# Optimization experiments

Hardware: AMD Instinct MI355X
Metric: run time of the kernel (lower is better)

## Reference

```python
import jax, jax.numpy as jnp
import numpy as np

D_MODEL = 256
N_HEAD = 8


def setup_inputs() -> dict:
    key = jax.random.key(0)
    ks = jax.random.split(key, 9)
    B, S, D = 2, 2048, D_MODEL
    s = 1.0 / np.sqrt(D)
    return {
        "x": jax.random.normal(ks[0], (B, S, D), dtype=jnp.float32),
        "wq": jax.random.uniform(ks[1], (D, D), jnp.float32, -s, s),
        "bq": jax.random.uniform(ks[2], (D,), jnp.float32, -s, s),
        "wk": jax.random.uniform(ks[3], (D, D), jnp.float32, -s, s),
        "bk": jax.random.uniform(ks[4], (D,), jnp.float32, -s, s),
        "wv": jax.random.uniform(ks[5], (D, D), jnp.float32, -s, s),
        "bv": jax.random.uniform(ks[6], (D,), jnp.float32, -s, s),
        "wc": jax.random.uniform(ks[7], (D, D), jnp.float32, -s, s),
        "bc": jax.random.uniform(ks[8], (D,), jnp.float32, -s, s),
    }


def _split_heads(t):
    # [B, S, D] -> [B, H, S, D/H]
    B, S, D = t.shape
    return t.reshape(B, S, N_HEAD, D // N_HEAD).transpose(0, 2, 1, 3)


def reference(x, wq, bq, wk, bk, wv, bv, wc, bc):
    q = _split_heads(x @ wq.T + bq)
    k = _split_heads(x @ wk.T + bk)
    v = _split_heads(x @ wv.T + bv)
    d_head = q.shape[-1]
    # full [B, H, S, S] score matrix, as in the original (non-fused)
    score = jnp.einsum("bhqd,bhkd->bhqk", q, k) / jnp.sqrt(jnp.float32(d_head))
    attn = jax.nn.softmax(score, axis=-1)
    out = jnp.einsum("bhqk,bhkd->bhqd", attn, v)
    B, H, S, Dh = out.shape
    out = out.transpose(0, 2, 1, 3).reshape(B, S, H * Dh)
    out = out @ wc.T + bc
    attention = jnp.mean(attn, axis=1)  # [B, S, S]
    return (out, attention)
```

## Files before the change

kernel.cpp:

```cpp
#include <hip/hip_runtime.h>
#include <hip/hip_bf16.h>


#define B_   2
#define S_   2048
#define D_   256
#define H_   8
#define DH_  32
#define NROW (B_*S_)
#define KSPLIT 4
#define KKEYS (S_/KSPLIT)

typedef __attribute__((ext_vector_type(8))) short bf16x8;
typedef __attribute__((ext_vector_type(4))) float f32x4;

__device__ __forceinline__ f32x4 mfma_bf16(bf16x8 a, bf16x8 b, f32x4 c) {
    return __builtin_amdgcn_mfma_f32_16x16x32_bf16(a, b, c, 0, 0, 0);
}

__device__ __forceinline__ float fast_exp2(float x) {
    return __builtin_amdgcn_exp2f(x);
}

__device__ __forceinline__ unsigned short f2bf_bits(float v) {
    __hip_bfloat16 h = __float2bfloat16(v);
    return *reinterpret_cast<unsigned short*>(&h);
}

__device__ __forceinline__ size_t fragidx(int m, int k) {
    return (size_t)(m >> 4) * 4096 + (k >> 5) * 512 + ((k >> 3) & 3) * 128
           + (m & 15) * 8 + (k & 7);
}

__global__ void split_all(const float4* __restrict__ x,
                          const float4* __restrict__ wq, const float4* __restrict__ wk,
                          const float4* __restrict__ wv, const float4* __restrict__ wc,
                          ushort4* __restrict__ xh, ushort4* __restrict__ xl,
                          ushort4* __restrict__ wqh, ushort4* __restrict__ wql,
                          ushort4* __restrict__ wkh, ushort4* __restrict__ wkl,
                          ushort4* __restrict__ wvh, ushort4* __restrict__ wvl,
                          ushort4* __restrict__ wch, ushort4* __restrict__ wcl) {
    int i = blockIdx.x * 256 + threadIdx.x;
    const float4* src; ushort4 *ph, *pl; int off;
    if (i < 262144) { src = x; ph = xh; pl = xl; off = i; }
    else {
        int j = i - 262144;
        int rg = j >> 14; off = j & 16383;
        if (rg == 0)      { src = wq; ph = wqh; pl = wql; }
        else if (rg == 1) { src = wk; ph = wkh; pl = wkl; }
        else if (rg == 2) { src = wv; ph = wvh; pl = wvl; }
        else              { src = wc; ph = wch; pl = wcl; }
    }
    float4 v = src[off];
    float vv[4] = {v.x, v.y, v.z, v.w};
    ushort4 hb, lb;
    unsigned short* hp = (unsigned short*)&hb;
    unsigned short* lp = (unsigned short*)&lb;
    for (int c = 0; c < 4; c++) {
        __hip_bfloat16 h = __float2bfloat16(vv[c]);
        hp[c] = *reinterpret_cast<unsigned short*>(&h);
        lp[c] = f2bf_bits(vv[c] - __bfloat162float(h));
    }
    int m = off >> 6, k = (off & 63) * 4;
    size_t fi = fragidx(m, k);
    ph[fi >> 2] = hb;
    pl[fi >> 2] = lb;
}

__global__ __launch_bounds__(256) void qkv_gemm(
    const __hip_bfloat16* __restrict__ xh, const __hip_bfloat16* __restrict__ xl,
    const __hip_bfloat16* __restrict__ w0h, const __hip_bfloat16* __restrict__ w0l,
    const __hip_bfloat16* __restrict__ w1h, const __hip_bfloat16* __restrict__ w1l,
    const __hip_bfloat16* __restrict__ w2h, const __hip_bfloat16* __restrict__ w2l,
    const float* __restrict__ bq, const float* __restrict__ bk, const float* __restrict__ bvv,
    __hip_bfloat16* __restrict__ Qf, __hip_bfloat16* __restrict__ Kf,
    __hip_bfloat16* __restrict__ Vf)
{
    int z = blockIdx.z;
    const __hip_bfloat16* wh = (z==0) ? w0h : (z==1) ? w1h : w2h;
    const __hip_bfloat16* wl = (z==0) ? w0l : (z==1) ? w1l : w2l;
    const float* bias = (z==0) ? bq : (z==1) ? bk : bvv;
    const float sv = (z==0) ? 0.17677669529663687f * 1.4426950408889634f : 1.0f;

    int tid = threadIdx.x;
    int w = tid >> 6, lid = tid & 63, quad = lid >> 4, l15 = lid & 15;
    int row0 = blockIdx.x * 64 + (w >> 1) * 32;
    int col0 = blockIdx.y * 64 + (w & 1) * 32;

    f32x4 acc[2][2] = {};
#pragma unroll
    for (int k0 = 0; k0 < 256; k0 += 32) {
        bf16x8 ah[2], al[2], bh[2], bl[2];
        for (int mi = 0; mi < 2; mi++) {
            size_t ro = (size_t)((row0 + mi * 16) >> 4) * 4096 + (k0 >> 5) * 512 + lid * 8;
            ah[mi] = *(const bf16x8*)(xh + ro);
            al[mi] = *(const bf16x8*)(xl + ro);
        }
        for (int ni = 0; ni < 2; ni++) {
            size_t co = (size_t)((col0 + ni * 16) >> 4) * 4096 + (k0 >> 5) * 512 + lid * 8;
            bh[ni] = *(const bf16x8*)(wh + co);
            bl[ni] = *(const bf16x8*)(wl + co);
        }
        for (int mi = 0; mi < 2; mi++)
            for (int ni = 0; ni < 2; ni++) {
                acc[mi][ni] = mfma_bf16(ah[mi], bh[ni], acc[mi][ni]);
                acc[mi][ni] = mfma_bf16(ah[mi], bl[ni], acc[mi][ni]);
                acc[mi][ni] = mfma_bf16(al[mi], bh[ni], acc[mi][ni]);
            }
    }
    for (int mi = 0; mi < 2; mi++)
        for (int ni = 0; ni < 2; ni++) {
            int col = col0 + ni * 16 + l15;
            int h = col >> 5, dh = col & 31;
            float bvl = bias[col];
            for (int r = 0; r < 4; r++) {
                int row = row0 + mi * 16 + quad * 4 + r;
                int b = row >> 11, s = row & 2047;
                __hip_bfloat16 o = __float2bfloat16((acc[mi][ni][r] + bvl) * sv);
                size_t bh_base = (size_t)(b * H_ + h) * (S_ * DH_);
                if (z == 2) {
                    int oo = s & 31;
                    int slot = ((oo & 15) >> 2) * 8 + ((oo >> 4) << 2) + (oo & 3);
                    Vf[bh_base + (s >> 5) * 1024 + (dh >> 4) * 512
                       + (slot >> 3) * 128 + (dh & 15) * 8 + (slot & 7)] = o;
                } else {
                    size_t idx = bh_base + (s >> 4) * 512 + (dh >> 3) * 128
                                 + (s & 15) * 8 + (dh & 7);
                    if (z == 0) Qf[idx] = o; else Kf[idx] = o;
                }
            }
        }
}

__global__ __launch_bounds__(256) void attn_flash(
    const __hip_bfloat16* __restrict__ Qf, const __hip_bfloat16* __restrict__ Kf,
    const __hip_bfloat16* __restrict__ Vf,
    float* __restrict__ Opart, float* __restrict__ Lpart)
{
    int tid = threadIdx.x, w = tid >> 6, lid = tid & 63, quad = lid >> 4, l15 = lid & 15;
    int h = blockIdx.y;
    int b = blockIdx.z >> 2, ks = blockIdx.z & 3;
    int q0 = (blockIdx.x * 4 + w) * 16;
    size_t bh_base = (size_t)(b * H_ + h) * (S_ * DH_);
    const __hip_bfloat16* Qp = Qf + bh_base + (q0 >> 4) * 512 + lid * 8;
    const __hip_bfloat16* Kp = Kf + bh_base + lid * 8;
    const __hip_bfloat16* Vp = Vf + bh_base + lid * 8;
    bf16x8 qf = *(const bf16x8*)Qp;
    f32x4 zacc = {};
    f32x4 oacc[2] = {};
    float lp0 = 0.f, lp1 = 0.f;

    int kbeg = ks * KKEYS;
    bf16x8 kf0 = *(const bf16x8*)(Kp + (kbeg >> 4) * 512);
    bf16x8 kf1 = *(const bf16x8*)(Kp + (kbeg >> 4) * 512 + 512);
    bf16x8 vf0 = *(const bf16x8*)(Vp + (kbeg >> 5) * 1024);
    bf16x8 vf1 = *(const bf16x8*)(Vp + (kbeg >> 5) * 1024 + 512);

#pragma unroll 2
    for (int k0 = kbeg; k0 < kbeg + KKEYS; k0 += 32) {
        bf16x8 ck0 = kf0, ck1 = kf1, cv0 = vf0, cv1 = vf1;
        int kn = (k0 + 32 < kbeg + KKEYS) ? k0 + 32 : kbeg;
        kf0 = *(const bf16x8*)(Kp + (kn >> 4) * 512);
        kf1 = *(const bf16x8*)(Kp + (kn >> 4) * 512 + 512);
        vf0 = *(const bf16x8*)(Vp + (kn >> 5) * 1024);
        vf1 = *(const bf16x8*)(Vp + (kn >> 5) * 1024 + 512);

        __builtin_amdgcn_s_setprio(1);
        f32x4 c0 = mfma_bf16(ck0, qf, zacc);
        f32x4 c1 = mfma_bf16(ck1, qf, zacc);
        __builtin_amdgcn_s_setprio(0);
        float e0[4], e1[4];
        for (int r = 0; r < 4; r++) {
            e0[r] = fast_exp2(c0[r]);
            e1[r] = fast_exp2(c1[r]);
        }
        lp0 += e0[0] + e0[1] + e0[2] + e0[3];
        lp1 += e1[0] + e1[1] + e1[2] + e1[3];
        union { bf16x8 v; __hip_bfloat162 h2[4]; } pu;
        pu.h2[0] = __float22bfloat162_rn(make_float2(e0[0], e0[1]));
        pu.h2[1] = __float22bfloat162_rn(make_float2(e0[2], e0[3]));
        pu.h2[2] = __float22bfloat162_rn(make_float2(e1[0], e1[1]));
        pu.h2[3] = __float22bfloat162_rn(make_float2(e1[2], e1[3]));
        __builtin_amdgcn_s_setprio(1);
        oacc[0] = mfma_bf16(cv0, pu.v, oacc[0]);
        oacc[1] = mfma_bf16(cv1, pu.v, oacc[1]);
        __builtin_amdgcn_s_setprio(0);
    }
    float lp = lp0 + lp1;
    lp += __shfl_xor(lp, 16);
    lp += __shfl_xor(lp, 32);

    size_t base = (size_t)((b * H_ + h) * KSPLIT + ks) * S_;
    if (lid < 16) Lpart[base + q0 + lid] = lp;
    f32x4* op = (f32x4*)(Opart + (base + q0 + l15) * DH_);
    op[quad] = oacc[0];
    op[quad + 4] = oacc[1];
}

__global__ __launch_bounds__(256) void attn_combine(
    const float* __restrict__ Opart, const float* __restrict__ Lpart,
    __hip_bfloat16* __restrict__ cth, __hip_bfloat16* __restrict__ ctl,
    float* __restrict__ invL)
{
    int i = blockIdx.x * 256 + threadIdx.x;
    int dh = i & 31;
    int s = (i >> 5) & (S_ - 1);
    int hb = i >> 16;
    float l = 0.f, o = 0.f;
#pragma unroll
    for (int ks = 0; ks < KSPLIT; ks++) {
        size_t base = (size_t)(hb * KSPLIT + ks) * S_ + s;
        l += Lpart[base];
        o += Opart[base * DH_ + dh];
    }
    float inv = 1.0f / l;
    float val = o * inv;
    int b = hb >> 3, h = hb & 7;
    size_t fi = fragidx(b * S_ + s, h * DH_ + dh);
    __hip_bfloat16 hv = __float2bfloat16(val);
    cth[fi] = hv;
    ctl[fi] = __float2bfloat16(val - __bfloat162float(hv));
    if (dh == 0) invL[hb * S_ + s] = inv;
}

__global__ __launch_bounds__(256) void attn_write(
    const __hip_bfloat16* __restrict__ Qf, const __hip_bfloat16* __restrict__ Kf,
    const float* __restrict__ invL, float* __restrict__ attn)
{
    __shared__ float invbuf[H_ * 16];
    int tid = threadIdx.x, w = tid >> 6, lid = tid & 63, quad = lid >> 4, l15 = lid & 15;
    int b = blockIdx.z;
    int q0 = blockIdx.y * 16;
    int k0 = blockIdx.x * 256 + w * 64;
    if (tid < 128) {
        int h = tid >> 4, r = tid & 15;
        invbuf[tid] = invL[(b * H_ + h) * S_ + q0 + r] * 0.125f;
    }
    __syncthreads();
    f32x4 zacc = {};
    float psum[4][4] = {};
    size_t bh0 = (size_t)b * H_ * (S_ * DH_);
    size_t qoff = (size_t)(q0 >> 4) * 512 + lid * 8;
    size_t koff = (size_t)(k0 >> 4) * 512 + lid * 8;

    bf16x8 qcur = *(const bf16x8*)(Qf + bh0 + qoff);
    bf16x8 kcur0 = *(const bf16x8*)(Kf + bh0 + koff);
    bf16x8 kcur1 = *(const bf16x8*)(Kf + bh0 + koff + 512);
    bf16x8 kcur2 = *(const bf16x8*)(Kf + bh0 + koff + 1024);
    bf16x8 kcur3 = *(const bf16x8*)(Kf + bh0 + koff + 1536);

#pragma unroll 2
    for (int h = 0; h < H_; h++) {
        int hn = (h < H_ - 1) ? h + 1 : h;
        size_t nb = bh0 + (size_t)hn * (S_ * DH_);
        bf16x8 qn = *(const bf16x8*)(Qf + nb + qoff);
        bf16x8 kn0 = *(const bf16x8*)(Kf + nb + koff);
        bf16x8 kn1 = *(const bf16x8*)(Kf + nb + koff + 512);
        bf16x8 kn2 = *(const bf16x8*)(Kf + nb + koff + 1024);
        bf16x8 kn3 = *(const bf16x8*)(Kf + nb + koff + 1536);

        float il[4];
        for (int r = 0; r < 4; r++) il[r] = invbuf[h * 16 + quad * 4 + r];

        __builtin_amdgcn_s_setprio(1);
        f32x4 c0 = mfma_bf16(qcur, kcur0, zacc);
        f32x4 c1 = mfma_bf16(qcur, kcur1, zacc);
        f32x4 c2 = mfma_bf16(qcur, kcur2, zacc);
        f32x4 c3 = mfma_bf16(qcur, kcur3, zacc);
        __builtin_amdgcn_s_setprio(0);
        for (int r = 0; r < 4; r++) {
            psum[0][r] += fast_exp2(c0[r]) * il[r];
            psum[1][r] += fast_exp2(c1[r]) * il[r];
            psum[2][r] += fast_exp2(c2[r]) * il[r];
            psum[3][r] += fast_exp2(c3[r]) * il[r];
        }
        qcur = qn;
        kcur0 = kn0; kcur1 = kn1; kcur2 = kn2; kcur3 = kn3;
    }
    for (int nt = 0; nt < 4; nt++)
        for (int r = 0; r < 4; r++)
            attn[(size_t)(b * S_ + q0 + quad * 4 + r) * S_ + k0 + nt * 16 + l15] =
                psum[nt][r];
}

__global__ __launch_bounds__(256) void out_gemm(
    const __hip_bfloat16* __restrict__ ch, const __hip_bfloat16* __restrict__ cl,
    const __hip_bfloat16* __restrict__ wh, const __hip_bfloat16* __restrict__ wl,
    const float* __restrict__ bias, float* __restrict__ out)
{
    int tid = threadIdx.x;
    int w = tid >> 6, lid = tid & 63, quad = lid >> 4, l15 = lid & 15;
    int row0 = blockIdx.x * 64 + (w >> 1) * 32;
    int col0 = blockIdx.y * 64 + (w & 1) * 32;

    f32x4 acc[2][2] = {};
#pragma unroll
    for (int k0 = 0; k0 < 256; k0 += 32) {
        bf16x8 ah[2], al[2], bh[2], bl[2];
        for (int mi = 0; mi < 2; mi++) {
            size_t ro = (size_t)((row0 + mi * 16) >> 4) * 4096 + (k0 >> 5) * 512 + lid * 8;
            ah[mi] = *(const bf16x8*)(ch + ro);
            al[mi] = *(const bf16x8*)(cl + ro);
        }
        for (int ni = 0; ni < 2; ni++) {
            size_t co = (size_t)((col0 + ni * 16) >> 4) * 4096 + (k0 >> 5) * 512 + lid * 8;
            bh[ni] = *(const bf16x8*)(wh + co);
            bl[ni] = *(const bf16x8*)(wl + co);
        }
        for (int mi = 0; mi < 2; mi++)
            for (int ni = 0; ni < 2; ni++) {
                acc[mi][ni] = mfma_bf16(ah[mi], bh[ni], acc[mi][ni]);
                acc[mi][ni] = mfma_bf16(ah[mi], bl[ni], acc[mi][ni]);
                acc[mi][ni] = mfma_bf16(al[mi], bh[ni], acc[mi][ni]);
            }
    }
    for (int mi = 0; mi < 2; mi++)
        for (int ni = 0; ni < 2; ni++) {
            int col = col0 + ni * 16 + l15;
            float bvl = bias[col];
            for (int r = 0; r < 4; r++) {
                int row = row0 + mi * 16 + quad * 4 + r;
                out[(size_t)row * 256 + col] = acc[mi][ni][r] + bvl;
            }
        }
}

extern "C" void kernel_launch(void* const* d_in, const int* in_sizes, int n_in,
                              void* d_out, int out_size, void* d_ws, size_t ws_size,
                              hipStream_t stream) {
    const float* x  = (const float*)d_in[0];
    const float* wq = (const float*)d_in[1];
    const float* bq = (const float*)d_in[2];
    const float* wk = (const float*)d_in[3];
    const float* bk = (const float*)d_in[4];
    const float* wv = (const float*)d_in[5];
    const float* bv = (const float*)d_in[6];
    const float* wc = (const float*)d_in[7];
    const float* bc = (const float*)d_in[8];

    char* ws = (char*)d_ws;
    const size_t MB = 1u << 20;
    const size_t KB128 = 128u * 1024u;
    __hip_bfloat16* xh  = (__hip_bfloat16*)(ws + 0 * MB);
    __hip_bfloat16* xl  = (__hip_bfloat16*)(ws + 2 * MB);
    __hip_bfloat16* wqh = (__hip_bfloat16*)(ws + 4 * MB + 0 * KB128);
    __hip_bfloat16* wql = (__hip_bfloat16*)(ws + 4 * MB + 1 * KB128);
    __hip_bfloat16* wkh = (__hip_bfloat16*)(ws + 4 * MB + 2 * KB128);
    __hip_bfloat16* wkl = (__hip_bfloat16*)(ws + 4 * MB + 3 * KB128);
    __hip_bfloat16* wvh = (__hip_bfloat16*)(ws + 4 * MB + 4 * KB128);
    __hip_bfloat16* wvl = (__hip_bfloat16*)(ws + 4 * MB + 5 * KB128);
    __hip_bfloat16* wch = (__hip_bfloat16*)(ws + 4 * MB + 6 * KB128);
    __hip_bfloat16* wcl = (__hip_bfloat16*)(ws + 4 * MB + 7 * KB128);
    __hip_bfloat16* Qfb = (__hip_bfloat16*)(ws + 5 * MB);
    __hip_bfloat16* Kfb = (__hip_bfloat16*)(ws + 7 * MB);
    __hip_bfloat16* Vfb = (__hip_bfloat16*)(ws + 9 * MB);
    __hip_bfloat16* cth = (__hip_bfloat16*)(ws + 11 * MB);
    __hip_bfloat16* ctl = (__hip_bfloat16*)(ws + 13 * MB);
    float* Opart = (float*)(ws + 15 * MB);
    float* Lpart = (float*)(ws + 31 * MB);
    float* invL  = (float*)(ws + 31 * MB + 512 * 1024);

    float* outp  = (float*)d_out;
    float* attnp = outp + (size_t)NROW * D_;

    hipLaunchKernelGGL(split_all, dim3(1280), dim3(256), 0, stream,
                       (const float4*)x, (const float4*)wq, (const float4*)wk,
                       (const float4*)wv, (const float4*)wc,
                       (ushort4*)xh, (ushort4*)xl,
                       (ushort4*)wqh, (ushort4*)wql, (ushort4*)wkh, (ushort4*)wkl,
                       (ushort4*)wvh, (ushort4*)wvl, (ushort4*)wch, (ushort4*)wcl);

    hipLaunchKernelGGL(qkv_gemm, dim3(NROW / 64, 4, 3), dim3(256), 0, stream,
                       xh, xl, wqh, wql, wkh, wkl, wvh, wvl, bq, bk, bv, Qfb, Kfb, Vfb);

    hipLaunchKernelGGL(attn_flash, dim3(S_ / 64, H_, B_ * KSPLIT), dim3(256), 0, stream,
                       Qfb, Kfb, Vfb, Opart, Lpart);

    hipLaunchKernelGGL(attn_combine, dim3(4096), dim3(256), 0, stream,
                       Opart, Lpart, cth, ctl, invL);

    hipLaunchKernelGGL(attn_write, dim3(S_ / 256, S_ / 16, B_), dim3(256), 0, stream,
                       Qfb, Kfb, invL, attnp);

    hipLaunchKernelGGL(out_gemm, dim3(NROW / 64, 4), dim3(256), 0, stream,
                       cth, ctl, wch, wcl, bc, outp);
}
```

Before: 142.4 us.

## Fuse split-K combine into flash kernel and merge attn-write with output GEMM

Each flash block now handles 16 queries with its four waves splitting the keys, and reduces the partial O and L through shared memory inside the block. This removes the Opart/Lpart global round trip and the separate combine kernel. The attention-map write and the output projection GEMM are merged into one launch by indexing on block ID, which cuts launch count and lets the two independent workloads overlap. The cost is a block-wide sync in the flash kernel and a heterogeneous grid whose two block types have different register needs.

```diff
diff --git a/kernel.cpp b/kernel.cpp
--- a/kernel.cpp
+++ b/kernel.cpp
@@ -135,12 +135,15 @@
 __global__ __launch_bounds__(256) void attn_flash(
     const __hip_bfloat16* __restrict__ Qf, const __hip_bfloat16* __restrict__ Kf,
     const __hip_bfloat16* __restrict__ Vf,
-    float* __restrict__ Opart, float* __restrict__ Lpart)
+    __hip_bfloat16* __restrict__ cth, __hip_bfloat16* __restrict__ ctl,
+    float* __restrict__ invL)
 {
+    __shared__ float sO[KSPLIT][16][33];
+    __shared__ float sL[KSPLIT][16];
     int tid = threadIdx.x, w = tid >> 6, lid = tid & 63, quad = lid >> 4, l15 = lid & 15;
     int h = blockIdx.y;
-    int b = blockIdx.z >> 2, ks = blockIdx.z & 3;
-    int q0 = (blockIdx.x * 4 + w) * 16;
+    int b = blockIdx.z;
+    int q0 = blockIdx.x * 16;
     size_t bh_base = (size_t)(b * H_ + h) * (S_ * DH_);
     const __hip_bfloat16* Qp = Qf + bh_base + (q0 >> 4) * 512 + lid * 8;
     const __hip_bfloat16* Kp = Kf + bh_base + lid * 8;
@@ -150,7 +153,7 @@
     f32x4 oacc[2] = {};
     float lp0 = 0.f, lp1 = 0.f;
 
-    int kbeg = ks * KKEYS;
+    int kbeg = w * KKEYS;
     bf16x8 kf0 = *(const bf16x8*)(Kp + (kbeg >> 4) * 512);
     bf16x8 kf1 = *(const bf16x8*)(Kp + (kbeg >> 4) * 512 + 512);
     bf16x8 vf0 = *(const bf16x8*)(Vp + (kbeg >> 5) * 1024);
@@ -190,139 +193,129 @@
     lp += __shfl_xor(lp, 16);
     lp += __shfl_xor(lp, 32);
 
-    size_t base = (size_t)((b * H_ + h) * KSPLIT + ks) * S_;
-    if (lid < 16) Lpart[base + q0 + lid] = lp;
-    f32x4* op = (f32x4*)(Opart + (base + q0 + l15) * DH_);
-    op[quad] = oacc[0];
-    op[quad + 4] = oacc[1];
-}
-
-__global__ __launch_bounds__(256) void attn_combine(
-    const float* __restrict__ Opart, const float* __restrict__ Lpart,
-    __hip_bfloat16* __restrict__ cth, __hip_bfloat16* __restrict__ ctl,
-    float* __restrict__ invL)
-{
-    int i = blockIdx.x * 256 + threadIdx.x;
-    int dh = i & 31;
-    int s = (i >> 5) & (S_ - 1);
-    int hb = i >> 16;
-    float l = 0.f, o = 0.f;
+    for (int r = 0; r < 4; r++) {
+        sO[w][l15][quad * 4 + r]      = oacc[0][r];
+        sO[w][l15][16 + quad * 4 + r] = oacc[1][r];
+    }
+    if (lid < 16) sL[w][lid] = lp;
+    __syncthreads();
+
+    int d = tid & 31, q = tid >> 5;
 #pragma unroll
-    for (int ks = 0; ks < KSPLIT; ks++) {
-        size_t base = (size_t)(hb * KSPLIT + ks) * S_ + s;
-        l += Lpart[base];
-        o += Opart[base * DH_ + dh];
-    }
-    float inv = 1.0f / l;
-    float val = o * inv;
-    int b = hb >> 3, h = hb & 7;
-    size_t fi = fragidx(b * S_ + s, h * DH_ + dh);
-    __hip_bfloat16 hv = __float2bfloat16(val);
-    cth[fi] = hv;
-    ctl[fi] = __float2bfloat16(val - __bfloat162float(hv));
-    if (dh == 0) invL[hb * S_ + s] = inv;
-}
-
-__global__ __launch_bounds__(256) void attn_write(
+    for (int qq = q; qq < 16; qq += 8) {
+        float l = sL[0][qq] + sL[1][qq] + sL[2][qq] + sL[3][qq];
+        float o = sO[0][qq][d] + sO[1][qq][d] + sO[2][qq][d] + sO[3][qq][d];
+        float inv = 1.0f / l;
+        float val = o * inv;
+        size_t fi = fragidx(b * S_ + q0 + qq, h * DH_ + d);
+        __hip_bfloat16 hv = __float2bfloat16(val);
+        cth[fi] = hv;
+        ctl[fi] = __float2bfloat16(val - __bfloat162float(hv));
+        if (d == 0) invL[(b * H_ + h) * S_ + q0 + qq] = inv;
+    }
+}
+
+__global__ __launch_bounds__(256) void attn_out(
     const __hip_bfloat16* __restrict__ Qf, const __hip_bfloat16* __restrict__ Kf,
-    const float* __restrict__ invL, float* __restrict__ attn)
+    const float* __restrict__ invL,
+    const __hip_bfloat16* __restrict__ ch, const __hip_bfloat16* __restrict__ cl,
+    const __hip_bfloat16* __restrict__ wh, const __hip_bfloat16* __restrict__ wl,
+    const float* __restrict__ bias,
+    float* __restrict__ attn, float* __restrict__ out)
 {
     __shared__ float invbuf[H_ * 16];
+    int bid = blockIdx.x;
     int tid = threadIdx.x, w = tid >> 6, lid = tid & 63, quad = lid >> 4, l15 = lid & 15;
-    int b = blockIdx.z;
-    int q0 = blockIdx.y * 16;
-    int k0 = blockIdx.x * 256 + w * 64;
-    if (tid < 128) {
-        int h = tid >> 4, r = tid & 15;
-        invbuf[tid] = invL[(b * H_ + h) * S_ + q0 + r] * 0.125f;
-    }
-    __syncthreads();
-    f32x4 zacc = {};
-    float psum[4][4] = {};
-    size_t bh0 = (size_t)b * H_ * (S_ * DH_);
-    size_t qoff = (size_t)(q0 >> 4) * 512 + lid * 8;
-    size_t koff = (size_t)(k0 >> 4) * 512 + lid * 8;
-
-    bf16x8 qcur = *(const bf16x8*)(Qf + bh0 + qoff);
-    bf16x8 kcur0 = *(const bf16x8*)(Kf + bh0 + koff);
-    bf16x8 kcur1 = *(const bf16x8*)(Kf + bh0 + koff + 512);
-    bf16x8 kcur2 = *(const bf16x8*)(Kf + bh0 + koff + 1024);
-    bf16x8 kcur3 = *(const bf16x8*)(Kf + bh0 + koff + 1536);
-
-#pragma unroll 2
-    for (int h = 0; h < H_; h++) {
-        int hn = (h < H_ - 1) ? h + 1 : h;
-        size_t nb = bh0 + (size_t)hn * (S_ * DH_);
-        bf16x8 qn = *(const bf16x8*)(Qf + nb + qoff);
-        bf16x8 kn0 = *(const bf16x8*)(Kf + nb + koff);
-        bf16x8 kn1 = *(const bf16x8*)(Kf + nb + koff + 512);
-        bf16x8 kn2 = *(const bf16x8*)(Kf + nb + koff + 1024);
-        bf16x8 kn3 = *(const bf16x8*)(Kf + nb + koff + 1536);
-
-        float il[4];
-        for (int r = 0; r < 4; r++) il[r] = invbuf[h * 16 + quad * 4 + r];
-
-        __builtin_amdgcn_s_setprio(1);
-        f32x4 c0 = mfma_bf16(qcur, kcur0, zacc);
-        f32x4 c1 = mfma_bf16(qcur, kcur1, zacc);
-        f32x4 c2 = mfma_bf16(qcur, kcur2, zacc);
-        f32x4 c3 = mfma_bf16(qcur, kcur3, zacc);
-        __builtin_amdgcn_s_setprio(0);
-        for (int r = 0; r < 4; r++) {
-            psum[0][r] += fast_exp2(c0[r]) * il[r];
-            psum[1][r] += fast_exp2(c1[r]) * il[r];
-            psum[2][r] += fast_exp2(c2[r]) * il[r];
-            psum[3][r] += fast_exp2(c3[r]) * il[r];
-        }
-        qcur = qn;
-        kcur0 = kn0; kcur1 = kn1; kcur2 = kn2; kcur3 = kn3;
-    }
-    for (int nt = 0; nt < 4; nt++)
-        for (int r = 0; r < 4; r++)
-            attn[(size_t)(b * S_ + q0 + quad * 4 + r) * S_ + k0 + nt * 16 + l15] =
-                psum[nt][r];
-}
-
-__global__ __launch_bounds__(256) void out_gemm(
-    const __hip_bfloat16* __restrict__ ch, const __hip_bfloat16* __restrict__ cl,
-    const __hip_bfloat16* __restrict__ wh, const __hip_bfloat16* __restrict__ wl,
-    const float* __restrict__ bias, float* __restrict__ out)
-{
-    int tid = threadIdx.x;
-    int w = tid >> 6, lid = tid & 63, quad = lid >> 4, l15 = lid & 15;
-    int row0 = blockIdx.x * 64 + (w >> 1) * 32;
-    int col0 = blockIdx.y * 64 + (w & 1) * 32;
-
-    f32x4 acc[2][2] = {};
+
+    if (bid < 256) {
+        int row0 = (bid & 63) * 64 + (w >> 1) * 32;
+        int col0 = (bid >> 6) * 64 + (w & 1) * 32;
+
+        f32x4 acc[2][2] = {};
 #pragma unroll
-    for (int k0 = 0; k0 < 256; k0 += 32) {
-        bf16x8 ah[2], al[2], bh[2], bl[2];
-        for (int mi = 0; mi < 2; mi++) {
-            size_t ro = (size_t)((row0 + mi * 16) >> 4) * 4096 + (k0 >> 5) * 512 + lid * 8;
-            ah[mi] = *(const bf16x8*)(ch + ro);
-            al[mi] = *(const bf16x8*)(cl + ro);
-        }
-        for (int ni = 0; ni < 2; ni++) {
-            size_t co = (size_t)((col0 + ni * 16) >> 4) * 4096 + (k0 >> 5) * 512 + lid * 8;
-            bh[ni] = *(const bf16x8*)(wh + co);
-            bl[ni] = *(const bf16x8*)(wl + co);
+        for (int k0 = 0; k0 < 256; k0 += 32) {
+            bf16x8 ah[2], al[2], bh[2], bl[2];
+            for (int mi = 0; mi < 2; mi++) {
+                size_t ro = (size_t)((row0 + mi * 16) >> 4) * 4096 + (k0 >> 5) * 512 + lid * 8;
+                ah[mi] = *(const bf16x8*)(ch + ro);
+                al[mi] = *(const bf16x8*)(cl + ro);
+            }
+            for (int ni = 0; ni < 2; ni++) {
+                size_t co = (size_t)((col0 + ni * 16) >> 4) * 4096 + (k0 >> 5) * 512 + lid * 8;
+                bh[ni] = *(const bf16x8*)(wh + co);
+                bl[ni] = *(const bf16x8*)(wl + co);
+            }
+            for (int mi = 0; mi < 2; mi++)
+                for (int ni = 0; ni < 2; ni++) {
+                    acc[mi][ni] = mfma_bf16(ah[mi], bh[ni], acc[mi][ni]);
+                    acc[mi][ni] = mfma_bf16(ah[mi], bl[ni], acc[mi][ni]);
+                    acc[mi][ni] = mfma_bf16(al[mi], bh[ni], acc[mi][ni]);
+                }
         }
         for (int mi = 0; mi < 2; mi++)
             for (int ni = 0; ni < 2; ni++) {
-                acc[mi][ni] = mfma_bf16(ah[mi], bh[ni], acc[mi][ni]);
-                acc[mi][ni] = mfma_bf16(ah[mi], bl[ni], acc[mi][ni]);
-                acc[mi][ni] = mfma_bf16(al[mi], bh[ni], acc[mi][ni]);
-            }
-    }
-    for (int mi = 0; mi < 2; mi++)
-        for (int ni = 0; ni < 2; ni++) {
-            int col = col0 + ni * 16 + l15;
-            float bvl = bias[col];
+                int col = col0 + ni * 16 + l15;
+                float bvl = bias[col];
+                for (int r = 0; r < 4; r++) {
+                    int row = row0 + mi * 16 + quad * 4 + r;
+                    out[(size_t)row * 256 + col] = acc[mi][ni][r] + bvl;
+                }
+            }
+    } else {
+        int ab = bid - 256;
+        int kx = ab & 7, qy = (ab >> 3) & 127, b = ab >> 10;
+        int q0 = qy * 16;
+        int k0 = kx * 256 + w * 64;
+        if (tid < 128) {
+            int h = tid >> 4, r = tid & 15;
+            invbuf[tid] = invL[(b * H_ + h) * S_ + q0 + r] * 0.125f;
+        }
+        __syncthreads();
+        f32x4 zacc = {};
+        float psum[4][4] = {};
+        size_t bh0 = (size_t)b * H_ * (S_ * DH_);
+        size_t qoff = (size_t)(q0 >> 4) * 512 + lid * 8;
+        size_t koff = (size_t)(k0 >> 4) * 512 + lid * 8;
+
+        bf16x8 qcur = *(const bf16x8*)(Qf + bh0 + qoff);
+        bf16x8 kcur0 = *(const bf16x8*)(Kf + bh0 + koff);
+        bf16x8 kcur1 = *(const bf16x8*)(Kf + bh0 + koff + 512);
+        bf16x8 kcur2 = *(const bf16x8*)(Kf + bh0 + koff + 1024);
+        bf16x8 kcur3 = *(const bf16x8*)(Kf + bh0 + koff + 1536);
+
+#pragma unroll 2
+        for (int h = 0; h < H_; h++) {
+            int hn = (h < H_ - 1) ? h + 1 : h;
+            size_t nb = bh0 + (size_t)hn * (S_ * DH_);
+            bf16x8 qn = *(const bf16x8*)(Qf + nb + qoff);
+            bf16x8 kn0 = *(const bf16x8*)(Kf + nb + koff);
+            bf16x8 kn1 = *(const bf16x8*)(Kf + nb + koff + 512);
+            bf16x8 kn2 = *(const bf16x8*)(Kf + nb + koff + 1024);
+            bf16x8 kn3 = *(const bf16x8*)(Kf + nb + koff + 1536);
+
+            float il[4];
+            for (int r = 0; r < 4; r++) il[r] = invbuf[h * 16 + quad * 4 + r];
+
+            __builtin_amdgcn_s_setprio(1);
+            f32x4 c0 = mfma_bf16(qcur, kcur0, zacc);
+            f32x4 c1 = mfma_bf16(qcur, kcur1, zacc);
+            f32x4 c2 = mfma_bf16(qcur, kcur2, zacc);
+            f32x4 c3 = mfma_bf16(qcur, kcur3, zacc);
+            __builtin_amdgcn_s_setprio(0);
             for (int r = 0; r < 4; r++) {
-                int row = row0 + mi * 16 + quad * 4 + r;
-                out[(size_t)row * 256 + col] = acc[mi][ni][r] + bvl;
-            }
-        }
+                psum[0][r] += fast_exp2(c0[r]) * il[r];
+                psum[1][r] += fast_exp2(c1[r]) * il[r];
+                psum[2][r] += fast_exp2(c2[r]) * il[r];
+                psum[3][r] += fast_exp2(c3[r]) * il[r];
+            }
+            qcur = qn;
+            kcur0 = kn0; kcur1 = kn1; kcur2 = kn2; kcur3 = kn3;
+        }
+        for (int nt = 0; nt < 4; nt++)
+            for (int r = 0; r < 4; r++)
+                attn[(size_t)(b * S_ + q0 + quad * 4 + r) * S_ + k0 + nt * 16 + l15] =
+                    psum[nt][r];
+    }
 }
 
 extern "C" void kernel_launch(void* const* d_in, const int* in_sizes, int n_in,
@@ -356,9 +349,7 @@
     __hip_bfloat16* Vfb = (__hip_bfloat16*)(ws + 9 * MB);
     __hip_bfloat16* cth = (__hip_bfloat16*)(ws + 11 * MB);
     __hip_bfloat16* ctl = (__hip_bfloat16*)(ws + 13 * MB);
-    float* Opart = (float*)(ws + 15 * MB);
-    float* Lpart = (float*)(ws + 31 * MB);
-    float* invL  = (float*)(ws + 31 * MB + 512 * 1024);
+    float* invL  = (float*)(ws + 15 * MB);
 
     float* outp  = (float*)d_out;
     float* attnp = outp + (size_t)NROW * D_;
@@ -373,15 +364,9 @@
     hipLaunchKernelGGL(qkv_gemm, dim3(NROW / 64, 4, 3), dim3(256), 0, stream,
                        xh, xl, wqh, wql, wkh, wkl, wvh, wvl, bq, bk, bv, Qfb, Kfb, Vfb);
 
-    hipLaunchKernelGGL(attn_flash, dim3(S_ / 64, H_, B_ * KSPLIT), dim3(256), 0, stream,
-                       Qfb, Kfb, Vfb, Opart, Lpart);
-
-    hipLaunchKernelGGL(attn_combine, dim3(4096), dim3(256), 0, stream,
-                       Opart, Lpart, cth, ctl, invL);
-
-    hipLaunchKernelGGL(attn_write, dim3(S_ / 256, S_ / 16, B_), dim3(256), 0, stream,
-                       Qfb, Kfb, invL, attnp);
-
-    hipLaunchKernelGGL(out_gemm, dim3(NROW / 64, 4), dim3(256), 0, stream,
-                       cth, ctl, wch, wcl, bc, outp);
-}
+    hipLaunchKernelGGL(attn_flash, dim3(S_ / 16, H_, B_), dim3(256), 0, stream,
+                       Qfb, Kfb, Vfb, cth, ctl, invL);
+
+    hipLaunchKernelGGL(attn_out, dim3(256 + 2048), dim3(256), 0, stream,
+                       Qfb, Kfb, invL, cth, ctl, wch, wcl, bc, attnp, outp);
+}
```

Measured after the change: 135.6 us. 1.05x faster.
